# Kernel tuning notes

Hardware: AMD Instinct MI355X
Metric: run time of the kernel (lower is better)

## Reference

```python
import jax, jax.numpy as jnp
import numpy as np

NEIGH_RADIUS = 1
NEIGH_DILATION = 1
NB_ITER = 3
GROUP_NB = 4
SOFTMAX_FACT = 1.0
EPS = 1e-8


def _directions():
    # matches computeNeighborsCoord: (x, y) pairs, row-major over y then x, center removed
    r = NEIGH_RADIUS
    return [(x * NEIGH_DILATION, y * NEIGH_DILATION)
            for y in range(-r, r + 1) for x in range(-r, r + 1)
            if not (x == 0 and y == 0)]


def _shift(feat, dx, dy):
    # out[..., i, j] = feat[..., i+dy, j+dx], zero outside the image; mask marks valid positions
    H, W = feat.shape[2], feat.shape[3]
    shifted = jnp.roll(feat, shift=(-dy, -dx), axis=(2, 3))
    vy = (np.arange(H) + dy >= 0) & (np.arange(H) + dy < H)
    vx = (np.arange(W) + dx >= 0) & (np.arange(W) + dx < W)
    mask = jnp.asarray(np.outer(vy, vx).astype(np.float32))[None, None]  # [1,1,H,W]
    return shifted * mask, mask


def _cossim(a, b):
    # channel-wise cosine similarity -> [B,1,H,W]
    num = jnp.sum(a * b, axis=1, keepdims=True)
    den = jnp.sqrt(jnp.sum(a * a, axis=1, keepdims=True)) * jnp.sqrt(jnp.sum(b * b, axis=1, keepdims=True))
    return num / jnp.maximum(den, EPS)


def _total_sim(feat, dirs):
    # mask-normalized mean cosine similarity with the 8 neighbors -> [B,1,H,W]
    num = 0.0
    cnt = 0.0
    for dx, dy in dirs:
        fs, m = _shift(feat, dx, dy)
        num = num + _cossim(feat, fs) * m
        cnt = cnt + m
    return num / cnt


def setup_inputs() -> dict:
    key = jax.random.key(0)
    features = jax.random.normal(key, (8, 32, 256, 256), dtype=jnp.float32)
    return {"features": features}


def reference(features):
    dirs = _directions()
    sim_maps = [_total_sim(features, dirs)]
    for _ in range(NB_ITER):
        sims = []
        fshifts = []
        for dx, dy in dirs:
            fs, m = _shift(features, dx, dy)
            sims.append(_cossim(features, fs) * m)  # masked sim, zeros at invalid positions
            fshifts.append(fs)                       # already masked shift
        all_sim = jax.nn.softmax(SOFTMAX_FACT * jnp.concatenate(sims, axis=1), axis=1)  # [B,8,H,W]
        new_feat = sum(all_sim[:, i:i + 1] * fshifts[i] for i in range(len(dirs)))       # [B,C,H,W]
        sim_maps.append(_total_sim(features, dirs))  # NOTE: pre-update features, as in original
        new_feat = new_feat / jnp.sum(all_sim, axis=1, keepdims=True)  # == conv2d with ones(1,8,1,1)
        features = new_feat
    out = jnp.concatenate(sim_maps, axis=1)  # [B, nbIter+1, H, W]
    B, T, H, W = out.shape
    out = out.reshape(B // GROUP_NB, GROUP_NB, T, H, W).mean(axis=1)
    return out
```

## Files before the change

### kernel.cpp

```cpp
#include <hip/hip_runtime.h>
#include <hip/hip_fp16.h>

#define HH 256
#define WW 256
#define CC 32
#define HWSZ (HH * WW)
#define IMGSZ (CC * HWSZ)
#define NIMG 8
#define EPSV 1e-8f
#define NCH (CC / 2)

__device__ __forceinline__ void acc_pass1(const float v[3][6],
                                          float sq[3][6], float dotv[8][4])
{
#pragma unroll
    for (int r = 0; r < 3; ++r)
#pragma unroll
        for (int j = 0; j < 6; ++j) sq[r][j] = fmaf(v[r][j], v[r][j], sq[r][j]);
    int d = 0;
#pragma unroll
    for (int dyi = 0; dyi < 3; ++dyi)
#pragma unroll
        for (int dxi = 0; dxi < 3; ++dxi) {
            if (dyi == 1 && dxi == 1) continue;
#pragma unroll
            for (int i = 0; i < 4; ++i)
                dotv[d][i] = fmaf(v[1][i + 1], v[dyi][i + dxi], dotv[d][i]);
            ++d;
        }
}

__device__ __forceinline__ void acc_pass2(const float v[3][6],
                                          const float w[8][4], float o[4])
{
    int d = 0;
#pragma unroll
    for (int dyi = 0; dyi < 3; ++dyi)
#pragma unroll
        for (int dxi = 0; dxi < 3; ++dxi) {
            if (dyi == 1 && dxi == 1) continue;
#pragma unroll
            for (int i = 0; i < 4; ++i)
                o[i] = fmaf(w[d][i], v[dyi][i + dxi], o[i]);
            ++d;
        }
}

__device__ __forceinline__ void gload16(const void* g, void* l)
{
    __builtin_amdgcn_global_load_lds(
        (const __attribute__((address_space(1))) void*)g,
        (__attribute__((address_space(3))) void*)l, 16, 0, 0);
}

__device__ __forceinline__ float cvtlo(unsigned u)
{ return __half2float(__ushort_as_half((unsigned short)(u & 0xffffu))); }
__device__ __forceinline__ float cvthi(unsigned u)
{ return __half2float(__ushort_as_half((unsigned short)(u >> 16))); }
__device__ __forceinline__ unsigned pkh(float a, float b)
{
    return (unsigned)__half_as_ushort(__float2half_rn(a)) |
           ((unsigned)__half_as_ushort(__float2half_rn(b)) << 16);
}

#define WAITB(VM) { asm volatile("s_waitcnt vmcnt(" #VM ")" ::: "memory"); \
                    __builtin_amdgcn_s_barrier(); }


#define STAGE(SLOT) { \
    const int ch_ = (SLOT) & 15; \
    const int bo_ = ((SLOT) & 3) * 8192; \
    gload16(gsrc0 + (size_t)ch_ * HWSZ,        ldst0 + bo_); \
    gload16(gsrc0 + (size_t)(ch_ + 16) * HWSZ, ldst0 + bo_ + 4096); }

#define LOADV(G, VV) { \
    const char* sp_ = slabb + ((G) & 3) * 8192; \
    _Pragma("unroll") \
    for (int r_ = 0; r_ < 3; ++r_) { \
        float4 m_ = *(const float4*)(sp_ + bM + r_ * 1024); \
        float e_ = 0.f; \
        if (edge) e_ = *(const float*)(sp_ + bE + r_ * 1024); \
        const float lu_ = __shfl_up(m_.w, 1); \
        const float rd_ = __shfl_down(m_.x, 1); \
        const bool ok_ = rowok[r_]; \
        VV[r_][0] = (ok_ && xl) ? ((tx == 0)  ? e_ : lu_) : 0.f; \
        VV[r_][1] = ok_ ? m_.x : 0.f; \
        VV[r_][2] = ok_ ? m_.y : 0.f; \
        VV[r_][3] = ok_ ? m_.z : 0.f; \
        VV[r_][4] = ok_ ? m_.w : 0.f; \
        VV[r_][5] = (ok_ && xr) ? ((tx == 31) ? e_ : rd_) : 0.f; \
    } }

template <bool YEDGE>
__device__ __forceinline__ void step1_body(const float* __restrict__ F,
                                           unsigned short* __restrict__ Fn,
                                           float* __restrict__ simout,
                                           char* slabb, int b, int rowblk, int tid)
{
    const int wave = tid >> 6;
    const int lane = tid & 63;
    const int half = lane >> 5;
    const int tx   = lane & 31;
    const int y0   = rowblk * 2;
    const int y    = y0 + (wave >> 1);
    const int x0   = (wave & 1) * 128 + (tx << 2);
    const int c0   = half * NCH;

    const bool ym = YEDGE ? (y > 0) : true;
    const bool yp = YEDGE ? (y < HH - 1) : true;
    const bool xl = x0 > 0, xr = x0 < WW - 4;
    const bool rowok[3] = { ym, true, yp };
    const bool colok[6] = { xl, true, true, true, true, xr };

    const float* Fb = F + (size_t)b * IMGSZ;
    int arow = y0 - 1 + wave;
    if (YEDGE) arow = arow < 0 ? 0 : (arow > HH - 1 ? HH - 1 : arow);
    const float* gsrc0 = Fb + arow * WW + (lane << 2);
    char* ldst0 = slabb + wave * 1024;

    const int rbase = half * 4096 + (wave >> 1) * 1024;
    const int bM = rbase + x0 * 4;
    const int bL = rbase + (xl ? x0 * 4 - 4 : 0);
    const int bR = rbase + (xr ? x0 * 4 + 16 : 1020);
    const bool edge = (tx == 0) || (tx == 31);
    const int bE = (tx == 31) ? bR : bL;

    float sq[3][6];
    float dotv[8][4];
#pragma unroll
    for (int r = 0; r < 3; ++r)
#pragma unroll
        for (int j = 0; j < 6; ++j) sq[r][j] = 0.f;
#pragma unroll
    for (int d = 0; d < 8; ++d)
#pragma unroll
        for (int i = 0; i < 4; ++i) dotv[d][i] = 0.f;

    STAGE(0) STAGE(1) STAGE(2)

#pragma unroll 1
    for (int g = 0; g < 16; ++g) {
        WAITB(4)
        STAGE(g + 3)
        float v[3][6];
        LOADV(g, v)
        acc_pass1(v, sq, dotv);
    }

#pragma unroll
    for (int r = 0; r < 3; ++r)
#pragma unroll
        for (int j = 0; j < 6; ++j) sq[r][j] += __shfl_xor(sq[r][j], 32);
#pragma unroll
    for (int d = 0; d < 8; ++d)
#pragma unroll
        for (int i = 0; i < 4; ++i) dotv[d][i] += __shfl_xor(dotv[d][i], 32);

    float nrm[3][6];
#pragma unroll
    for (int r = 0; r < 3; ++r)
#pragma unroll
        for (int j = 0; j < 6; ++j) nrm[r][j] = __builtin_amdgcn_sqrtf(sq[r][j]);

    float w[8][4];
    float simarr[4];
#pragma unroll
    for (int i = 0; i < 4; ++i) {
        float s[8];
        const float cn = nrm[1][i + 1];
        float tot = 0.f, cnt = 0.f;
        int d = 0;
#pragma unroll
        for (int dyi = 0; dyi < 3; ++dyi)
#pragma unroll
            for (int dxi = 0; dxi < 3; ++dxi) {
                if (dyi == 1 && dxi == 1) continue;
                const bool m = rowok[dyi] && colok[i + dxi];
                const float den = fmaxf(cn * nrm[dyi][i + dxi], EPSV);
                const float cs = dotv[d][i] * __builtin_amdgcn_rcpf(den);
                s[d] = m ? cs : 0.f;
                tot += s[d];
                cnt += m ? 1.f : 0.f;
                ++d;
            }
        simarr[i] = tot * __builtin_amdgcn_rcpf(cnt);
        {
            float mx = s[0];
#pragma unroll
            for (int d2 = 1; d2 < 8; ++d2) mx = fmaxf(mx, s[d2]);
            float wsum = 0.f;
#pragma unroll
            for (int d2 = 0; d2 < 8; ++d2) { w[d2][i] = __expf(s[d2] - mx); wsum += w[d2][i]; }
            const float inv = __builtin_amdgcn_rcpf(wsum);
#pragma unroll
            for (int d2 = 0; d2 < 8; ++d2) w[d2][i] *= inv;
        }
    }
    if (half == 0) {
        float4 simv = { simarr[0], simarr[1], simarr[2], simarr[3] };
        *reinterpret_cast<float4*>(simout + b * HWSZ + y * WW + x0) = simv;
    }

    {
        unsigned short* outp = Fn + (size_t)b * IMGSZ + (size_t)c0 * HWSZ + y * WW + x0;
#pragma unroll 1
        for (int g = 16; g < 29; ++g) {
            WAITB(4)
            STAGE(g + 3)
            float v[3][6];
            LOADV(g, v)
            float o[4] = { 0.f, 0.f, 0.f, 0.f };
            acc_pass2(v, w, o);
            uint2 ov; ov.x = pkh(o[0], o[1]); ov.y = pkh(o[2], o[3]);
            *reinterpret_cast<uint2*>(outp + (g & 15) * HWSZ) = ov;
        }
        { WAITB(4) float v[3][6]; LOADV(29, v)
          float o[4] = { 0.f, 0.f, 0.f, 0.f }; acc_pass2(v, w, o);
          uint2 ov; ov.x = pkh(o[0], o[1]); ov.y = pkh(o[2], o[3]);
          *reinterpret_cast<uint2*>(outp + 13 * HWSZ) = ov; }
        { WAITB(2) float v[3][6]; LOADV(30, v)
          float o[4] = { 0.f, 0.f, 0.f, 0.f }; acc_pass2(v, w, o);
          uint2 ov; ov.x = pkh(o[0], o[1]); ov.y = pkh(o[2], o[3]);
          *reinterpret_cast<uint2*>(outp + 14 * HWSZ) = ov; }
        { WAITB(0) float v[3][6]; LOADV(31, v)
          float o[4] = { 0.f, 0.f, 0.f, 0.f }; acc_pass2(v, w, o);
          uint2 ov; ov.x = pkh(o[0], o[1]); ov.y = pkh(o[2], o[3]);
          *reinterpret_cast<uint2*>(outp + 15 * HWSZ) = ov; }
    }
}

__global__ __launch_bounds__(256, 4) void step1_kernel(const float* __restrict__ F,
                                                       unsigned short* __restrict__ Fn,
                                                       float* __restrict__ simout)
{
    const int linear = blockIdx.y * (HH / 2) + blockIdx.x;
    const int remap  = (linear & 7) * 128 + (linear >> 3);
    const int b      = remap >> 7;
    const int rowblk = remap & 127;

    __shared__ float4 slab4[2048];

    if (rowblk != 0 && rowblk != 127)
        step1_body<false>(F, Fn, simout, (char*)slab4, b, rowblk, threadIdx.x);
    else
        step1_body<true>(F, Fn, simout, (char*)slab4, b, rowblk, threadIdx.x);
}


#define STAGE_H(SLOT) { \
    gload16(gsrcH + (size_t)(((SLOT) & 15) + halfS * 16) * HWSZ, \
            ldstH + ((SLOT) & 3) * 4096); }

#define LOADV_H(G, VV) { \
    const char* sp_ = slabb + ((G) & 3) * 4096; \
    _Pragma("unroll") \
    for (int r_ = 0; r_ < 3; ++r_) { \
        uint2 b_ = *(const uint2*)(sp_ + bMH + r_ * 512); \
        float e_ = 0.f; \
        if (edge && eok) { \
            unsigned eu_ = *(const unsigned*)(sp_ + bEH + r_ * 512); \
            e_ = (tx == 31) ? cvtlo(eu_) : cvthi(eu_); \
        } \
        const unsigned lu32_ = __shfl_up(b_.y, 1); \
        const unsigned rd32_ = __shfl_down(b_.x, 1); \
        const bool ok_ = rowok[r_]; \
        VV[r_][0] = (ok_ && xl) ? ((tx == 0)  ? e_ : cvthi(lu32_)) : 0.f; \
        VV[r_][1] = ok_ ? cvtlo(b_.x) : 0.f; \
        VV[r_][2] = ok_ ? cvthi(b_.x) : 0.f; \
        VV[r_][3] = ok_ ? cvtlo(b_.y) : 0.f; \
        VV[r_][4] = ok_ ? cvthi(b_.y) : 0.f; \
        VV[r_][5] = (ok_ && xr) ? ((tx == 31) ? e_ : cvtlo(rd32_)) : 0.f; \
    } }

template <bool YEDGE, bool COMPUTE_NEXT>
__device__ __forceinline__ void steph_body(const unsigned short* __restrict__ F,
                                           unsigned short* __restrict__ Fn,
                                           float* __restrict__ simout,
                                           char* slabb, int b, int rowblk, int tid)
{
    const int wave = tid >> 6;
    const int lane = tid & 63;
    const int half = lane >> 5;
    const int tx   = lane & 31;
    const int y0   = rowblk * 2;
    const int y    = y0 + (wave >> 1);
    const int x0   = (wave & 1) * 128 + (tx << 2);
    const int c0   = half * NCH;

    const bool ym = YEDGE ? (y > 0) : true;
    const bool yp = YEDGE ? (y < HH - 1) : true;
    const bool xl = x0 > 0, xr = x0 < WW - 4;
    const bool rowok[3] = { ym, true, yp };
    const bool colok[6] = { xl, true, true, true, true, xr };

    const unsigned short* Fb = F + (size_t)b * IMGSZ;

    const int halfS = wave >> 1;
    const int rp    = wave & 1;
    int srow = y0 - 1 + 2 * rp;
    int dsh  = 0;
    if (YEDGE) {
        if (srow < 0)            { srow = 0;      dsh = 512;  }
        else if (srow + 1 > HH - 1) { srow = HH - 2; dsh = -512; }
    }
    const unsigned short* gsrcH = Fb + srow * WW + lane * 8;
    char* ldstH = slabb + halfS * 2048 + rp * 1024 + dsh;

    const int bMH = half * 2048 + (wave >> 1) * 512 + x0 * 2;
    const bool edge = (tx == 0) || (tx == 31);
    const bool eok  = (tx == 31) ? xr : xl;
    const int bEH   = (tx == 31) ? (bMH + 8) : (bMH - 4);

    float sq[3][6];
    float dotv[8][4];
#pragma unroll
    for (int r = 0; r < 3; ++r)
#pragma unroll
        for (int j = 0; j < 6; ++j) sq[r][j] = 0.f;
#pragma unroll
    for (int d = 0; d < 8; ++d)
#pragma unroll
        for (int i = 0; i < 4; ++i) dotv[d][i] = 0.f;

    STAGE_H(0) STAGE_H(1) STAGE_H(2)

#pragma unroll 1
    for (int g = 0; g < (COMPUTE_NEXT ? 16 : 13); ++g) {
        WAITB(2)
        STAGE_H(g + 3)
        float v[3][6];
        LOADV_H(g, v)
        acc_pass1(v, sq, dotv);
    }
    if (!COMPUTE_NEXT) {
        { WAITB(2) float v[3][6]; LOADV_H(13, v) acc_pass1(v, sq, dotv); }
        { WAITB(1) float v[3][6]; LOADV_H(14, v) acc_pass1(v, sq, dotv); }
        { WAITB(0) float v[3][6]; LOADV_H(15, v) acc_pass1(v, sq, dotv); }
    }

#pragma unroll
    for (int r = 0; r < 3; ++r)
#pragma unroll
        for (int j = 0; j < 6; ++j) sq[r][j] += __shfl_xor(sq[r][j], 32);
#pragma unroll
    for (int d = 0; d < 8; ++d)
#pragma unroll
        for (int i = 0; i < 4; ++i) dotv[d][i] += __shfl_xor(dotv[d][i], 32);

    float nrm[3][6];
#pragma unroll
    for (int r = 0; r < 3; ++r)
#pragma unroll
        for (int j = 0; j < 6; ++j) nrm[r][j] = __builtin_amdgcn_sqrtf(sq[r][j]);

    float w[8][4];
    float simarr[4];
#pragma unroll
    for (int i = 0; i < 4; ++i) {
        float s[8];
        const float cn = nrm[1][i + 1];
        float tot = 0.f, cnt = 0.f;
        int d = 0;
#pragma unroll
        for (int dyi = 0; dyi < 3; ++dyi)
#pragma unroll
            for (int dxi = 0; dxi < 3; ++dxi) {
                if (dyi == 1 && dxi == 1) continue;
                const bool m = rowok[dyi] && colok[i + dxi];
                const float den = fmaxf(cn * nrm[dyi][i + dxi], EPSV);
                const float cs = dotv[d][i] * __builtin_amdgcn_rcpf(den);
                s[d] = m ? cs : 0.f;
                tot += s[d];
                cnt += m ? 1.f : 0.f;
                ++d;
            }
        simarr[i] = tot * __builtin_amdgcn_rcpf(cnt);
        if (COMPUTE_NEXT) {
            float mx = s[0];
#pragma unroll
            for (int d2 = 1; d2 < 8; ++d2) mx = fmaxf(mx, s[d2]);
            float wsum = 0.f;
#pragma unroll
            for (int d2 = 0; d2 < 8; ++d2) { w[d2][i] = __expf(s[d2] - mx); wsum += w[d2][i]; }
            const float inv = __builtin_amdgcn_rcpf(wsum);
#pragma unroll
            for (int d2 = 0; d2 < 8; ++d2) w[d2][i] *= inv;
        }
    }
    if (half == 0) {
        float4 simv = { simarr[0], simarr[1], simarr[2], simarr[3] };
        *reinterpret_cast<float4*>(simout + b * HWSZ + y * WW + x0) = simv;
    }

    if (COMPUTE_NEXT) {
        unsigned short* outp = Fn + (size_t)b * IMGSZ + (size_t)c0 * HWSZ + y * WW + x0;

#define PASS2H(VM, G) { \
            WAITB(VM) \
            if ((G) < 29) STAGE_H((G) + 3) \
            float v[3][6]; \
            LOADV_H(G, v) \
            float o[4] = { 0.f, 0.f, 0.f, 0.f }; \
            acc_pass2(v, w, o); \
            uint2 ov; ov.x = pkh(o[0], o[1]); ov.y = pkh(o[2], o[3]); \
            *reinterpret_cast<uint2*>(outp + ((G) & 15) * HWSZ) = ov; }

        PASS2H(3, 16)
        PASS2H(4, 17)
#pragma unroll 1
        for (int g = 18; g < 29; ++g) {
            PASS2H(5, g)
        }
        PASS2H(5, 29)
        PASS2H(4, 30)
        PASS2H(3, 31)
#undef PASS2H
    }
}

template <bool COMPUTE_NEXT>
__global__ __launch_bounds__(256, 4) void steph_kernel(const unsigned short* __restrict__ F,
                                                       unsigned short* __restrict__ Fn,
                                                       float* __restrict__ simout)
{
    const int linear = blockIdx.y * (HH / 2) + blockIdx.x;
    const int remap  = (linear & 7) * 128 + (linear >> 3);
    const int b      = remap >> 7;
    const int rowblk = remap & 127;

    __shared__ float4 slabH[1024];

    if (rowblk != 0 && rowblk != 127)
        steph_body<false, COMPUTE_NEXT>(F, Fn, simout, (char*)slabH, b, rowblk, threadIdx.x);
    else
        steph_body<true,  COMPUTE_NEXT>(F, Fn, simout, (char*)slabH, b, rowblk, threadIdx.x);
}

__global__ __launch_bounds__(256) void reduce_kernel(const float* __restrict__ sims,
                                                     float* __restrict__ out)
{
    const int idx = blockIdx.x * blockDim.x + threadIdx.x;
    const int p4 = idx & (HWSZ / 4 - 1);
    const int t  = (idx >> 14) & 3;
    const int g  = idx >> 16;
    const int tt = (t <= 1) ? 0 : (t - 1);
    const float4* s = reinterpret_cast<const float4*>(sims) +
                      (size_t)(tt * NIMG + g * 4) * (HWSZ / 4) + p4;
    float4 a = s[0];
    float4 b = s[HWSZ / 4];
    float4 c = s[2 * (HWSZ / 4)];
    float4 d = s[3 * (HWSZ / 4)];
    float4 o;
    o.x = 0.25f * (a.x + b.x + c.x + d.x);
    o.y = 0.25f * (a.y + b.y + c.y + d.y);
    o.z = 0.25f * (a.z + b.z + c.z + d.z);
    o.w = 0.25f * (a.w + b.w + c.w + d.w);
    reinterpret_cast<float4*>(out)[idx] = o;
}

extern "C" void kernel_launch(void* const* d_in, const int* in_sizes, int n_in,
                              void* d_out, int out_size, void* d_ws, size_t ws_size,
                              hipStream_t stream)
{
    const float* F0 = (const float*)d_in[0];
    unsigned short* F1h = (unsigned short*)d_ws;
    unsigned short* F2h = F1h + (size_t)NIMG * IMGSZ;
    float* sims = (float*)(F2h + (size_t)NIMG * IMGSZ);

    dim3 block(256);
    dim3 grid(HH / 2, NIMG);

    hipLaunchKernelGGL(step1_kernel,          grid, block, 0, stream, F0, F1h, sims);
    hipLaunchKernelGGL((steph_kernel<true>),  grid, block, 0, stream, F1h, F2h, sims + (size_t)NIMG * HWSZ);
    hipLaunchKernelGGL((steph_kernel<false>), grid, block, 0, stream, F2h, nullptr, sims + (size_t)2 * NIMG * HWSZ);

    hipLaunchKernelGGL(reduce_kernel, dim3((2 * 4 * HWSZ / 4) / 256), block, 0, stream,
                       sims, (float*)d_out);
}
```

Before: 98.96 us.

## Restructure fp16 stencil pipeline to stage channel pairs in triple-buffered LDS

The half-precision step kernel now stages two channels per pipeline step into a 3-slot LDS ring of 8 KB slots, instead of one channel per step into a 4-slot ring of 4 KB slots. Each wait is followed by two channel computations, and the next async load is issued after the compute rather than before it. This halves the number of barriers and waits per channel and deepens the prefetch. In exchange, LDS per block grows from 16 KB to 24 KB, which may reduce occupancy, and the wait-count bookkeeping is more intricate.

```diff
diff --git a/kernel.cpp b/kernel.cpp
--- a/kernel.cpp
+++ b/kernel.cpp
@@ -247,12 +247,13 @@
 }
 
 
-#define STAGE_H(SLOT) { \
-    gload16(gsrcH + (size_t)(((SLOT) & 15) + halfS * 16) * HWSZ, \
-            ldstH + ((SLOT) & 3) * 4096); }
-
-#define LOADV_H(G, VV) { \
-    const char* sp_ = slabb + ((G) & 3) * 4096; \
+#define STAGE_P(P) { \
+    const int ps_ = ((P) % 3) * 8192; \
+    gload16(gsrcH + (size_t)(2 * ((P) & 7)     + halfS * 16) * HWSZ, ldstH + ps_); \
+    gload16(gsrcH + (size_t)(2 * ((P) & 7) + 1 + halfS * 16) * HWSZ, ldstH + ps_ + 4096); }
+
+#define LOADV_H(SB, VV) { \
+    const char* sp_ = slabb + (SB); \
     _Pragma("unroll") \
     for (int r_ = 0; r_ < 3; ++r_) { \
         uint2 b_ = *(const uint2*)(sp_ + bMH + r_ * 512); \
@@ -300,7 +301,7 @@
     int srow = y0 - 1 + 2 * rp;
     int dsh  = 0;
     if (YEDGE) {
-        if (srow < 0)            { srow = 0;      dsh = 512;  }
+        if (srow < 0)               { srow = 0;      dsh = 512;  }
         else if (srow + 1 > HH - 1) { srow = HH - 2; dsh = -512; }
     }
     const unsigned short* gsrcH = Fb + srow * WW + lane * 8;
@@ -322,20 +323,23 @@
 #pragma unroll
         for (int i = 0; i < 4; ++i) dotv[d][i] = 0.f;
 
-    STAGE_H(0) STAGE_H(1) STAGE_H(2)
+    STAGE_P(0) STAGE_P(1)
 
 #pragma unroll 1
-    for (int g = 0; g < (COMPUTE_NEXT ? 16 : 13); ++g) {
+    for (int p = 0; p < (COMPUTE_NEXT ? 8 : 6); ++p) {
         WAITB(2)
-        STAGE_H(g + 3)
-        float v[3][6];
-        LOADV_H(g, v)
-        acc_pass1(v, sq, dotv);
+        const int sb = (p % 3) * 8192;
+        { float v[3][6]; LOADV_H(sb, v)        acc_pass1(v, sq, dotv); }
+        { float v[3][6]; LOADV_H(sb + 4096, v) acc_pass1(v, sq, dotv); }
+        STAGE_P(p + 2)
     }
     if (!COMPUTE_NEXT) {
-        { WAITB(2) float v[3][6]; LOADV_H(13, v) acc_pass1(v, sq, dotv); }
-        { WAITB(1) float v[3][6]; LOADV_H(14, v) acc_pass1(v, sq, dotv); }
-        { WAITB(0) float v[3][6]; LOADV_H(15, v) acc_pass1(v, sq, dotv); }
+        { WAITB(2) const int sb = 0;
+          float v[3][6]; LOADV_H(sb, v)        acc_pass1(v, sq, dotv);
+          { float u[3][6]; LOADV_H(sb + 4096, u) acc_pass1(u, sq, dotv); } }
+        { WAITB(0) const int sb = 8192;
+          float v[3][6]; LOADV_H(sb, v)        acc_pass1(v, sq, dotv);
+          { float u[3][6]; LOADV_H(sb + 4096, u) acc_pass1(u, sq, dotv); } }
     }
 
 #pragma unroll
@@ -395,26 +399,28 @@
     if (COMPUTE_NEXT) {
         unsigned short* outp = Fn + (size_t)b * IMGSZ + (size_t)c0 * HWSZ + y * WW + x0;
 
-#define PASS2H(VM, G) { \
-            WAITB(VM) \
-            if ((G) < 29) STAGE_H((G) + 3) \
-            float v[3][6]; \
-            LOADV_H(G, v) \
-            float o[4] = { 0.f, 0.f, 0.f, 0.f }; \
-            acc_pass2(v, w, o); \
-            uint2 ov; ov.x = pkh(o[0], o[1]); ov.y = pkh(o[2], o[3]); \
-            *reinterpret_cast<uint2*>(outp + ((G) & 15) * HWSZ) = ov; }
-
-        PASS2H(3, 16)
-        PASS2H(4, 17)
+#define PASS2_PAIR(P) { \
+            const int sb_ = ((P) % 3) * 8192; \
+            const int ch_ = 2 * ((P) & 7); \
+            { float v[3][6]; LOADV_H(sb_, v) \
+              float o[4] = { 0.f, 0.f, 0.f, 0.f }; acc_pass2(v, w, o); \
+              uint2 ov; ov.x = pkh(o[0], o[1]); ov.y = pkh(o[2], o[3]); \
+              *reinterpret_cast<uint2*>(outp + ch_ * HWSZ) = ov; } \
+            { float v[3][6]; LOADV_H(sb_ + 4096, v) \
+              float o[4] = { 0.f, 0.f, 0.f, 0.f }; acc_pass2(v, w, o); \
+              uint2 ov; ov.x = pkh(o[0], o[1]); ov.y = pkh(o[2], o[3]); \
+              *reinterpret_cast<uint2*>(outp + (ch_ + 1) * HWSZ) = ov; } }
+
+        { WAITB(3) PASS2_PAIR(8) STAGE_P(10) }
 #pragma unroll 1
-        for (int g = 18; g < 29; ++g) {
-            PASS2H(5, g)
-        }
-        PASS2H(5, 29)
-        PASS2H(4, 30)
-        PASS2H(3, 31)
-#undef PASS2H
+        for (int p = 9; p < 14; ++p) {
+            WAITB(4)
+            PASS2_PAIR(p)
+            STAGE_P(p + 2)
+        }
+        { WAITB(4) PASS2_PAIR(14) }
+        { WAITB(2) PASS2_PAIR(15) }
+#undef PASS2_PAIR
     }
 }
 
@@ -428,7 +434,7 @@
     const int b      = remap >> 7;
     const int rowblk = remap & 127;
 
-    __shared__ float4 slabH[1024];
+    __shared__ float4 slabH[1536];
 
     if (rowblk != 0 && rowblk != 127)
         steph_body<false, COMPUTE_NEXT>(F, Fn, simout, (char*)slabH, b, rowblk, threadIdx.x);
```

Result: faster. 96.15 us (-2.8%).
